# Kernel tuning notes

Hardware: AMD Instinct MI355X
Metric: run time of the kernel (lower is better)

Reference implementation:

```python
import jax, jax.numpy as jnp
import numpy as np

H, I, E, K = 1024, 2816, 8, 2  # hidden, intermediate, n_experts, topk
B, S = 2, 2048


def setup_inputs() -> dict:
    key = jax.random.key(0)
    ks = jax.random.split(key, 6)
    def init(k, shape, fan_in):
        return (jax.random.normal(k, shape, jnp.float32) / np.sqrt(fan_in)).astype(jnp.float32)
    return {
        "x": jax.random.normal(ks[0], (B, S, H), jnp.float32),
        "Wgate": init(ks[1], (H, E), H),   # gating Linear weight (in,out layout)
        "bgate": jnp.zeros((E,), jnp.float32),  # gating Linear bias (nn.Linear default bias=True)
        "Wg": init(ks[2], (E, H, I), H),   # stacked gate_proj, mlp_bias=False
        "Wu": init(ks[3], (E, H, I), H),   # stacked up_proj
        "Wd": init(ks[4], (E, I, H), I),   # stacked down_proj
    }


def reference(x, Wgate, bgate, Wg, Wu, Wd):
    Bb, Ss, Hd = x.shape
    xf = x.reshape(-1, Hd)                       # [N, H] flattened tokens
    logits = xf @ Wgate + bgate                  # [N, E] gate logits
    topv, topi = jax.lax.top_k(logits, K)        # [N, K]
    N = xf.shape[0]
    # sparse combine weights: raw top-k LOGITS (no softmax), zeros elsewhere
    # (faithful to torch: scatter of logits_topk into -inf mask; -inf slots
    #  are never read since only selected experts contribute)
    combine = jnp.zeros_like(logits).at[jnp.arange(N)[:, None], topi].set(topv)  # [N, E]
    # dense grouped SwiGLU over all experts, then sparse combine
    g = jnp.einsum('nh,ehi->nei', xf, Wg)        # [N, E, I]
    u = jnp.einsum('nh,ehi->nei', xf, Wu)        # [N, E, I]
    h = jax.nn.silu(g) * u                       # [N, E, I]
    eo = jnp.einsum('nei,eih->neh', h, Wd)       # [N, E, H]
    out = jnp.einsum('neh,ne->nh', eo, combine).reshape(Bb, Ss, Hd)
    return out, logits
```

## Files before the change

kernel.cpp:

```cpp
#include <hip/hip_runtime.h>

#define HDIM 1024
#define IDIM 2816
#define NEXP 8
#define NTOK 4096
#define NROWS 8192
#define RPAD 8320
#define MAXT 71
#define MAXT64 136
#define GU_NYT 44
#define GU_TG 8
#define GU_NTG 9
#define GU_NWG (GU_NTG * GU_NYT * GU_TG)
#define DN_NWG (MAXT64 * 8)
#define TLDP 130

typedef short bf16x8 __attribute__((ext_vector_type(8)));
typedef float f32x4 __attribute__((ext_vector_type(4)));
typedef unsigned short u16x8 __attribute__((ext_vector_type(8)));

static __device__ __forceinline__ float bf2f(unsigned int u) {
    union { unsigned int i; float f; } v; v.i = u << 16; return v.f;
}
static __device__ __forceinline__ unsigned short f2bf(float f) {
    union { float f; unsigned int i; } v; v.f = f;
    return (unsigned short)((v.i + 0x7fffu + ((v.i >> 16) & 1u)) >> 16);
}

static __device__ __forceinline__ void gload16(const void* g, void* l) {
    __builtin_amdgcn_global_load_lds(
        (const __attribute__((address_space(1))) unsigned int*)g,
        (__attribute__((address_space(3))) unsigned int*)l, 16, 0, 0);
}

__global__ __launch_bounds__(256) void gating_kernel(
    const float* __restrict__ x, const float* __restrict__ Wgate,
    const float* __restrict__ bgate, float* __restrict__ logits_out,
    int* __restrict__ counts, int* __restrict__ topi, float* __restrict__ topv)
{
    int wave = (blockIdx.x << 2) + (threadIdx.x >> 6);
    int lane = threadIdx.x & 63;
    if (wave >= NTOK) return;
    const float* xr = x + (size_t)wave * HDIM;

    double acc[NEXP];
#pragma unroll
    for (int e = 0; e < NEXP; ++e) acc[e] = 0.0;
    for (int it = 0; it < HDIM / 64; ++it) {
        int h = lane + (it << 6);
        float xv = xr[h];
        const float* wr = Wgate + (size_t)h * NEXP;
#pragma unroll
        for (int e = 0; e < NEXP; ++e) acc[e] += (double)xv * (double)wr[e];
    }
#pragma unroll
    for (int e = 0; e < NEXP; ++e) {
        double v = acc[e];
        for (int off = 32; off; off >>= 1) v += __shfl_xor(v, off, 64);
        acc[e] = v + (double)bgate[e];
    }
    float lf[NEXP];
#pragma unroll
    for (int e = 0; e < NEXP; ++e) lf[e] = (float)acc[e];

    if (lane < NEXP) logits_out[(size_t)wave * NEXP + lane] = lf[lane];

    if (lane == 0) {
        int i1 = 0; float v1 = lf[0];
#pragma unroll
        for (int e = 1; e < NEXP; ++e) if (lf[e] > v1) { v1 = lf[e]; i1 = e; }
        int i2 = -1; float v2 = -3.0e38f;
#pragma unroll
        for (int e = 0; e < NEXP; ++e) {
            if (e == i1) continue;
            if (lf[e] > v2) { v2 = lf[e]; i2 = e; }
        }
        topi[wave * 2 + 0] = i1; topv[wave * 2 + 0] = v1;
        topi[wave * 2 + 1] = i2; topv[wave * 2 + 1] = v2;
        atomicAdd(&counts[i1], 1);
        atomicAdd(&counts[i2], 1);
    }
}

__global__ void offsets_kernel(const int* __restrict__ counts,
                               int* __restrict__ offs, int* __restrict__ cursor,
                               int* __restrict__ ntile, int* __restrict__ te,
                               int* __restrict__ tm0,
                               int* __restrict__ ntile64, int* __restrict__ te64,
                               int* __restrict__ tm64)
{
    if (threadIdx.x == 0 && blockIdx.x == 0) {
        int s = 0;
        for (int e = 0; e < NEXP; ++e) { offs[e] = s; cursor[e] = s; s += counts[e]; }
        offs[NEXP] = s;
        int nt = 0, nt64 = 0;
        for (int e = 0; e < NEXP; ++e) {
            int c = counts[e], base = offs[e];
            for (int mt = 0; mt * 128 < c; ++mt) { te[nt] = e; tm0[nt] = base + mt * 128; ++nt; }
            for (int mt = 0; mt * 64 < c; ++mt) { te64[nt64] = e; tm64[nt64] = base + mt * 64; ++nt64; }
        }
        *ntile = nt;
        *ntile64 = nt64;
    }
}

__global__ __launch_bounds__(256) void scatter_kernel(
    const float* __restrict__ x, const int* __restrict__ topi,
    const float* __restrict__ topv, int* __restrict__ cursor,
    float* __restrict__ row_w, int* __restrict__ pos_of,
    unsigned short* __restrict__ Xg)
{
    int p = (blockIdx.x << 2) + (threadIdx.x >> 6);
    int lane = threadIdx.x & 63;
    if (p >= NROWS) return;
    int n = p >> 1;
    int e = topi[p];
    float w = topv[p];
    int pos = 0;
    if (lane == 0) {
        pos = atomicAdd(&cursor[e], 1);
        row_w[pos] = w;
        pos_of[p] = pos;
    }
    pos = __shfl(pos, 0, 64);
    const float* xr = x + (size_t)n * HDIM;
    unsigned short* dst = Xg + (size_t)pos * HDIM;
#pragma unroll
    for (int it = 0; it < HDIM / 256; ++it) {
        int idx = (it * 64 + lane) * 4;
        float4 v = *reinterpret_cast<const float4*>(&xr[idx]);
        ushort4 o;
        o.x = f2bf(v.x); o.y = f2bf(v.y); o.z = f2bf(v.z); o.w = f2bf(v.w);
        *reinterpret_cast<ushort4*>(&dst[idx]) = o;
    }
}

__global__ __launch_bounds__(256) void transpose_gu_kernel(
    const float* __restrict__ Wg, const float* __restrict__ Wu,
    unsigned short* __restrict__ W2)
{
    __shared__ unsigned short lds[128 * TLDP];
    const int kind = blockIdx.z;
    const int e = blockIdx.y;
    const int tt = blockIdx.x;
    const int tr = tt / 22, tc = tt % 22;
    const int tid = threadIdx.x;

    const float* s0 = (kind ? Wu : Wg) + (size_t)e * HDIM * IDIM;
    {
        int r = tid >> 1, ch = (tid & 1) * 64;
        const float* sp = s0 + (size_t)(tr * 128 + r) * IDIM + tc * 128 + ch;
        unsigned short* lp = &lds[r * TLDP + ch];
#pragma unroll
        for (int q = 0; q < 8; ++q) {
            float4 a = *reinterpret_cast<const float4*>(sp + q * 8);
            float4 b = *reinterpret_cast<const float4*>(sp + q * 8 + 4);
            u16x8 o;
            o[0] = f2bf(a.x); o[1] = f2bf(a.y); o[2] = f2bf(a.z); o[3] = f2bf(a.w);
            o[4] = f2bf(b.x); o[5] = f2bf(b.y); o[6] = f2bf(b.z); o[7] = f2bf(b.w);
            *reinterpret_cast<u16x8*>(lp + q * 8) = o;
        }
    }
    __syncthreads();
    {
        const int g = tid & 15;
        unsigned short* d0 = W2 + (size_t)e * 2 * IDIM * HDIM + tr * 128 + g * 8;
#pragma unroll
        for (int cb = 0; cb < 8; ++cb) {
            int c = cb * 16 + (tid >> 4);
            u16x8 o;
#pragma unroll
            for (int jj = 0; jj < 8; ++jj) o[jj] = lds[(g * 8 + jj) * TLDP + c];
            int i = tc * 128 + c;
            int r2 = ((i >> 4) << 5) + (kind << 4) + (i & 15);
            *reinterpret_cast<u16x8*>(d0 + (size_t)r2 * HDIM) = o;
        }
    }
}

__global__ __launch_bounds__(256) void transpose_d_kernel(
    const float* __restrict__ Wd, unsigned short* __restrict__ Wdt)
{
    __shared__ unsigned short lds[128 * TLDP];
    const int e = blockIdx.y;
    const int tt = blockIdx.x;
    const int tr = tt / 8, tc = tt % 8;
    const int tid = threadIdx.x;

    const float* s0 = Wd + (size_t)e * IDIM * HDIM;
    {
        int r = tid >> 1, ch = (tid & 1) * 64;
        const float* sp = s0 + (size_t)(tr * 128 + r) * HDIM + tc * 128 + ch;
        unsigned short* lp = &lds[r * TLDP + ch];
#pragma unroll
        for (int q = 0; q < 8; ++q) {
            float4 a = *reinterpret_cast<const float4*>(sp + q * 8);
            float4 b = *reinterpret_cast<const float4*>(sp + q * 8 + 4);
            u16x8 o;
            o[0] = f2bf(a.x); o[1] = f2bf(a.y); o[2] = f2bf(a.z); o[3] = f2bf(a.w);
            o[4] = f2bf(b.x); o[5] = f2bf(b.y); o[6] = f2bf(b.z); o[7] = f2bf(b.w);
            *reinterpret_cast<u16x8*>(lp + q * 8) = o;
        }
    }
    __syncthreads();
    {
        const int g = tid & 15;
        unsigned short* d0 = Wdt + (size_t)e * HDIM * IDIM + tr * 128 + g * 8;
#pragma unroll
        for (int cb = 0; cb < 8; ++cb) {
            int c = cb * 16 + (tid >> 4);
            u16x8 o;
#pragma unroll
            for (int jj = 0; jj < 8; ++jj) o[jj] = lds[(g * 8 + jj) * TLDP + c];
            *reinterpret_cast<u16x8*>(d0 + (size_t)(tc * 128 + c) * IDIM) = o;
        }
    }
}

__global__ __launch_bounds__(256, 4) void gateup_kernel(
    const unsigned short* __restrict__ Xg,
    const unsigned short* __restrict__ W2,
    const int* __restrict__ offs,
    const int* __restrict__ ntile, const int* __restrict__ te,
    const int* __restrict__ tm0, unsigned short* __restrict__ hbuf)
{
    __shared__ unsigned short As[128 * 64];
    __shared__ unsigned short Bs[128 * 64];

    int bid = blockIdx.x;
    int xcd = bid & 7, rest = bid >> 3;
    int wg = xcd * (GU_NWG / 8) + rest;
    int tg = wg / (GU_NYT * GU_TG);
    int r2 = wg % (GU_NYT * GU_TG);
    int ny = r2 >> 3, ti = r2 & 7;
    int t = tg * GU_TG + ti;
    if (t >= *ntile) return;

    const int e = te[t];
    const int m0 = tm0[t];
    const int r1 = offs[e + 1];
    const int n0 = ny * 128;

    const unsigned short* wb = W2 + (size_t)e * 2 * IDIM * HDIM;

    const int tid = threadIdx.x;
    const int lane = tid & 63, wv = tid >> 6;
    const int wr = (wv >> 1) * 64, wc = (wv & 1) * 64;
    const int lr = lane & 15, kq16 = lane >> 4;

    const int a_row8 = tid >> 3;
    const int a_c16 = tid & 7;

    f32x4 acc[4][4];
#pragma unroll
    for (int m = 0; m < 4; ++m)
#pragma unroll
        for (int n = 0; n < 4; ++n) acc[m][n] = {0.f, 0.f, 0.f, 0.f};

    for (int k0 = 0; k0 < HDIM; k0 += 64) {
        __syncthreads();
#pragma unroll
        for (int ch = 0; ch < 4; ++ch) {
            int row = ch * 32 + a_row8;
            int c16s = a_c16 ^ (row & 7);
            gload16(&Xg[(size_t)(m0 + row) * HDIM + k0 + c16s * 8], &As[ch * 2048 + tid * 8]);
            gload16(&wb[(size_t)(n0 + row) * HDIM + k0 + c16s * 8], &Bs[ch * 2048 + tid * 8]);
        }
        __syncthreads();

#pragma unroll
        for (int ks = 0; ks < 2; ++ks) {
            bf16x8 af[4], bf[4];
#pragma unroll
            for (int m = 0; m < 4; ++m) {
                int row = wr + m * 16 + lr;
                int sw = (ks * 4 + kq16) ^ (row & 7);
                af[m] = *reinterpret_cast<const bf16x8*>(&As[row * 64 + sw * 8]);
            }
#pragma unroll
            for (int n = 0; n < 4; ++n) {
                int row = wc + n * 16 + lr;
                int sw = (ks * 4 + kq16) ^ (row & 7);
                bf[n] = *reinterpret_cast<const bf16x8*>(&Bs[row * 64 + sw * 8]);
            }
#pragma unroll
            for (int m = 0; m < 4; ++m)
#pragma unroll
                for (int n = 0; n < 4; ++n)
                    acc[m][n] = __builtin_amdgcn_mfma_f32_16x16x32_bf16(af[m], bf[n], acc[m][n], 0, 0, 0);
        }
    }

    const int rr = (lane >> 4) * 4;
    const int iloc0 = ((wc >> 5) << 4) + lr;
    const int col0 = ny * 64 + iloc0;
#pragma unroll
    for (int m = 0; m < 4; ++m) {
#pragma unroll
        for (int j = 0; j < 4; ++j) {
            int grow = m0 + wr + m * 16 + rr + j;
            if (grow < r1) {
                unsigned short* hr = &hbuf[(size_t)grow * IDIM + col0];
                float g0 = acc[m][0][j], u0 = acc[m][1][j];
                float g1 = acc[m][2][j], u1 = acc[m][3][j];
                hr[0]  = f2bf(g0 / (1.0f + __expf(-g0)) * u0);
                hr[16] = f2bf(g1 / (1.0f + __expf(-g1)) * u1);
            }
        }
    }
}

__global__ __launch_bounds__(256, 4) void down_kernel(
    const unsigned short* __restrict__ hbuf,
    const unsigned short* __restrict__ Wdt,
    const int* __restrict__ offs,
    const int* __restrict__ ntile64, const int* __restrict__ te64,
    const int* __restrict__ tm64,
    const float* __restrict__ row_w,
    unsigned short* __restrict__ eobuf)
{
    __shared__ unsigned short As[64 * 64];
    __shared__ unsigned short Bs[128 * 64];

    int bid = blockIdx.x;
    int xcd = bid & 7, rest = bid >> 3;
    int ny = rest / 17;
    int t = xcd * 17 + rest % 17;
    if (t >= *ntile64) return;

    const int e = te64[t];
    const int m0 = tm64[t];
    const int r1 = offs[e + 1];
    const int n0 = ny * 128;

    const unsigned short* wd = Wdt + (size_t)e * HDIM * IDIM;

    const int tid = threadIdx.x;
    const int lane = tid & 63, wv = tid >> 6;
    const int wc = wv * 32;
    const int lr = lane & 15, kq16 = lane >> 4;

    const int a_row8 = tid >> 3;
    const int a_c16 = tid & 7;

    f32x4 acc[4][2];
#pragma unroll
    for (int m = 0; m < 4; ++m)
#pragma unroll
        for (int n = 0; n < 2; ++n) acc[m][n] = {0.f, 0.f, 0.f, 0.f};

    for (int k0 = 0; k0 < IDIM; k0 += 64) {
        __syncthreads();
#pragma unroll
        for (int ch = 0; ch < 2; ++ch) {
            int row = ch * 32 + a_row8;
            int c16s = a_c16 ^ (row & 7);
            gload16(&hbuf[(size_t)(m0 + row) * IDIM + k0 + c16s * 8], &As[ch * 2048 + tid * 8]);
        }
#pragma unroll
        for (int ch = 0; ch < 4; ++ch) {
            int row = ch * 32 + a_row8;
            int c16s = a_c16 ^ (row & 7);
            gload16(&wd[(size_t)(n0 + row) * IDIM + k0 + c16s * 8], &Bs[ch * 2048 + tid * 8]);
        }
        __syncthreads();

#pragma unroll
        for (int ks = 0; ks < 2; ++ks) {
            bf16x8 af[4], bf[2];
#pragma unroll
            for (int m = 0; m < 4; ++m) {
                int row = m * 16 + lr;
                int sw = (ks * 4 + kq16) ^ (row & 7);
                af[m] = *reinterpret_cast<const bf16x8*>(&As[row * 64 + sw * 8]);
            }
#pragma unroll
            for (int n = 0; n < 2; ++n) {
                int row = wc + n * 16 + lr;
                int sw = (ks * 4 + kq16) ^ (row & 7);
                bf[n] = *reinterpret_cast<const bf16x8*>(&Bs[row * 64 + sw * 8]);
            }
#pragma unroll
            for (int m = 0; m < 4; ++m)
#pragma unroll
                for (int n = 0; n < 2; ++n)
                    acc[m][n] = __builtin_amdgcn_mfma_f32_16x16x32_bf16(af[m], bf[n], acc[m][n], 0, 0, 0);
        }
    }

    const int rr = (lane >> 4) * 4;
#pragma unroll
    for (int m = 0; m < 4; ++m) {
#pragma unroll
        for (int j = 0; j < 4; ++j) {
            int grow = m0 + m * 16 + rr + j;
            if (grow < r1) {
                float w = row_w[grow];
                unsigned short* er = &eobuf[(size_t)grow * HDIM + n0 + wc + lr];
#pragma unroll
                for (int n = 0; n < 2; ++n)
                    er[n * 16] = f2bf(acc[m][n][j] * w);
            }
        }
    }
}

__global__ __launch_bounds__(256) void combine_kernel(
    const unsigned short* __restrict__ eobuf, const int* __restrict__ pos_of,
    float* __restrict__ out)
{
    int t = blockIdx.x * 256 + threadIdx.x;
    int n = t >> 7;
    int c = (t & 127) << 3;
    int p0 = pos_of[n * 2 + 0];
    int p1 = pos_of[n * 2 + 1];
    uint4 a = *reinterpret_cast<const uint4*>(&eobuf[(size_t)p0 * HDIM + c]);
    uint4 b = *reinterpret_cast<const uint4*>(&eobuf[(size_t)p1 * HDIM + c]);
    float4 o0, o1;
    o0.x = bf2f(a.x & 0xffffu) + bf2f(b.x & 0xffffu);
    o0.y = bf2f(a.x >> 16)     + bf2f(b.x >> 16);
    o0.z = bf2f(a.y & 0xffffu) + bf2f(b.y & 0xffffu);
    o0.w = bf2f(a.y >> 16)     + bf2f(b.y >> 16);
    o1.x = bf2f(a.z & 0xffffu) + bf2f(b.z & 0xffffu);
    o1.y = bf2f(a.z >> 16)     + bf2f(b.z >> 16);
    o1.z = bf2f(a.w & 0xffffu) + bf2f(b.w & 0xffffu);
    o1.w = bf2f(a.w >> 16)     + bf2f(b.w >> 16);
    float* op = out + (size_t)n * HDIM + c;
    *reinterpret_cast<float4*>(op) = o0;
    *reinterpret_cast<float4*>(op + 4) = o1;
}

extern "C" void kernel_launch(void* const* d_in, const int* in_sizes, int n_in,
                              void* d_out, int out_size, void* d_ws, size_t ws_size,
                              hipStream_t stream)
{
    const float* x     = (const float*)d_in[0];
    const float* Wgate = (const float*)d_in[1];
    const float* bgate = (const float*)d_in[2];
    const float* Wg    = (const float*)d_in[3];
    const float* Wu    = (const float*)d_in[4];
    const float* Wd    = (const float*)d_in[5];
    float* out = (float*)d_out;
    float* logits = out + (size_t)NTOK * HDIM;

    char* ws = (char*)d_ws;
    unsigned short* Xg   = (unsigned short*)ws;
    unsigned short* hbuf = (unsigned short*)(ws + 17039360);
    unsigned short* W2   = (unsigned short*)(ws + 63897600);
    char* meta = ws + 156172288;
    int*   counts  = (int*)(meta);
    int*   offs    = (int*)(meta + 64);
    int*   cursor  = (int*)(meta + 128);
    int*   ntile   = (int*)(meta + 192);
    int*   ntile64 = (int*)(meta + 196);
    int*   te      = (int*)(meta + 256);
    int*   tm0     = (int*)(meta + 768);
    int*   te64    = (int*)(meta + 1280);
    int*   tm64    = (int*)(meta + 2048);
    int*   topi    = (int*)(meta + 4096);
    float* topv    = (float*)(meta + 36864);
    float* row_w   = (float*)(meta + 69632);
    int*   pos_of  = (int*)(meta + 102400);

    hipMemsetAsync(counts, 0, 32, stream);

    gating_kernel<<<NTOK / 4, 256, 0, stream>>>(x, Wgate, bgate, logits, counts, topi, topv);
    offsets_kernel<<<1, 64, 0, stream>>>(counts, offs, cursor, ntile, te, tm0,
                                         ntile64, te64, tm64);
    scatter_kernel<<<NROWS / 4, 256, 0, stream>>>(x, topi, topv, cursor, row_w, pos_of, Xg);

    transpose_gu_kernel<<<dim3(176, NEXP, 2), 256, 0, stream>>>(Wg, Wu, W2);

    gateup_kernel<<<GU_NWG, 256, 0, stream>>>(Xg, W2, offs, ntile, te, tm0, hbuf);

    transpose_d_kernel<<<dim3(176, NEXP), 256, 0, stream>>>(Wd, W2);

    down_kernel<<<DN_NWG, 256, 0, stream>>>(hbuf, W2, offs, ntile64, te64, tm64,
                                            row_w, Xg );

    combine_kernel<<<NTOK * HDIM / 8 / 256, 256, 0, stream>>>(Xg, pos_of, out);
}
```

Baseline: 490.8 us.

## Use 128x128 tiles in down-proj GEMM and coalesce transpose tile reads

The down-projection kernel moves from 64-row M tiles to the 128-row tiles already built for gate/up, with a 2x2 wave layout where each wave computes a 64x64 sub-tile. This doubles reuse of each loaded Wd tile per block and halves the number of blocks, which removes the separate 64-row tile list. It also drops the XCD-aware block remap, costs more accumulator registers and LDS, and leaves fewer blocks to fill the GPU. Separately, the weight transpose kernels now read source tiles with fully coalesced float4 accesses spread across rows, replacing the per-thread half-row reads.

```diff
diff --git a/kernel.cpp b/kernel.cpp
--- a/kernel.cpp
+++ b/kernel.cpp
@@ -7,12 +7,11 @@
 #define NROWS 8192
 #define RPAD 8320
 #define MAXT 71
-#define MAXT64 136
 #define GU_NYT 44
 #define GU_TG 8
 #define GU_NTG 9
 #define GU_NWG (GU_NTG * GU_NYT * GU_TG)
-#define DN_NWG (MAXT64 * 8)
+#define DN_NWG (MAXT * 8)
 #define TLDP 130
 
 typedef short bf16x8 __attribute__((ext_vector_type(8)));
@@ -85,22 +84,18 @@
 __global__ void offsets_kernel(const int* __restrict__ counts,
                                int* __restrict__ offs, int* __restrict__ cursor,
                                int* __restrict__ ntile, int* __restrict__ te,
-                               int* __restrict__ tm0,
-                               int* __restrict__ ntile64, int* __restrict__ te64,
-                               int* __restrict__ tm64)
+                               int* __restrict__ tm0)
 {
     if (threadIdx.x == 0 && blockIdx.x == 0) {
         int s = 0;
         for (int e = 0; e < NEXP; ++e) { offs[e] = s; cursor[e] = s; s += counts[e]; }
         offs[NEXP] = s;
-        int nt = 0, nt64 = 0;
+        int nt = 0;
         for (int e = 0; e < NEXP; ++e) {
             int c = counts[e], base = offs[e];
             for (int mt = 0; mt * 128 < c; ++mt) { te[nt] = e; tm0[nt] = base + mt * 128; ++nt; }
-            for (int mt = 0; mt * 64 < c; ++mt) { te64[nt64] = e; tm64[nt64] = base + mt * 64; ++nt64; }
         }
         *ntile = nt;
-        *ntile64 = nt64;
     }
 }
 
@@ -135,6 +130,21 @@
     }
 }
 
+static __device__ __forceinline__ void tp_read_tile(
+    const float* __restrict__ sp, int C, int tid, unsigned short* lds)
+{
+#pragma unroll
+    for (int q = 0; q < 16; ++q) {
+        int idx = q * 1024 + tid * 4;
+        int r = idx >> 7, cc = idx & 127;
+        float4 v = *reinterpret_cast<const float4*>(sp + (size_t)r * C + cc);
+        unsigned w0 = (unsigned)f2bf(v.x) | ((unsigned)f2bf(v.y) << 16);
+        unsigned w1 = (unsigned)f2bf(v.z) | ((unsigned)f2bf(v.w) << 16);
+        unsigned* lp = reinterpret_cast<unsigned*>(&lds[r * TLDP + cc]);
+        lp[0] = w0; lp[1] = w1;
+    }
+}
+
 __global__ __launch_bounds__(256) void transpose_gu_kernel(
     const float* __restrict__ Wg, const float* __restrict__ Wu,
     unsigned short* __restrict__ W2)
@@ -147,20 +157,7 @@
     const int tid = threadIdx.x;
 
     const float* s0 = (kind ? Wu : Wg) + (size_t)e * HDIM * IDIM;
-    {
-        int r = tid >> 1, ch = (tid & 1) * 64;
-        const float* sp = s0 + (size_t)(tr * 128 + r) * IDIM + tc * 128 + ch;
-        unsigned short* lp = &lds[r * TLDP + ch];
-#pragma unroll
-        for (int q = 0; q < 8; ++q) {
-            float4 a = *reinterpret_cast<const float4*>(sp + q * 8);
-            float4 b = *reinterpret_cast<const float4*>(sp + q * 8 + 4);
-            u16x8 o;
-            o[0] = f2bf(a.x); o[1] = f2bf(a.y); o[2] = f2bf(a.z); o[3] = f2bf(a.w);
-            o[4] = f2bf(b.x); o[5] = f2bf(b.y); o[6] = f2bf(b.z); o[7] = f2bf(b.w);
-            *reinterpret_cast<u16x8*>(lp + q * 8) = o;
-        }
-    }
+    tp_read_tile(s0 + (size_t)(tr * 128) * IDIM + tc * 128, IDIM, tid, lds);
     __syncthreads();
     {
         const int g = tid & 15;
@@ -188,20 +185,7 @@
     const int tid = threadIdx.x;
 
     const float* s0 = Wd + (size_t)e * IDIM * HDIM;
-    {
-        int r = tid >> 1, ch = (tid & 1) * 64;
-        const float* sp = s0 + (size_t)(tr * 128 + r) * HDIM + tc * 128 + ch;
-        unsigned short* lp = &lds[r * TLDP + ch];
-#pragma unroll
-        for (int q = 0; q < 8; ++q) {
-            float4 a = *reinterpret_cast<const float4*>(sp + q * 8);
-            float4 b = *reinterpret_cast<const float4*>(sp + q * 8 + 4);
-            u16x8 o;
-            o[0] = f2bf(a.x); o[1] = f2bf(a.y); o[2] = f2bf(a.z); o[3] = f2bf(a.w);
-            o[4] = f2bf(b.x); o[5] = f2bf(b.y); o[6] = f2bf(b.z); o[7] = f2bf(b.w);
-            *reinterpret_cast<u16x8*>(lp + q * 8) = o;
-        }
-    }
+    tp_read_tile(s0 + (size_t)(tr * 128) * HDIM + tc * 128, HDIM, tid, lds);
     __syncthreads();
     {
         const int g = tid & 15;
@@ -314,22 +298,21 @@
     const unsigned short* __restrict__ hbuf,
     const unsigned short* __restrict__ Wdt,
     const int* __restrict__ offs,
-    const int* __restrict__ ntile64, const int* __restrict__ te64,
-    const int* __restrict__ tm64,
+    const int* __restrict__ ntile, const int* __restrict__ te,
+    const int* __restrict__ tm0,
     const float* __restrict__ row_w,
     unsigned short* __restrict__ eobuf)
 {
-    __shared__ unsigned short As[64 * 64];
+    __shared__ unsigned short As[128 * 64];
     __shared__ unsigned short Bs[128 * 64];
 
     int bid = blockIdx.x;
-    int xcd = bid & 7, rest = bid >> 3;
-    int ny = rest / 17;
-    int t = xcd * 17 + rest % 17;
-    if (t >= *ntile64) return;
-
-    const int e = te64[t];
-    const int m0 = tm64[t];
+    int ny = bid & 7;
+    int t = bid >> 3;
+    if (t >= *ntile) return;
+
+    const int e = te[t];
+    const int m0 = tm0[t];
     const int r1 = offs[e + 1];
     const int n0 = ny * 128;
 
@@ -337,45 +320,40 @@
 
     const int tid = threadIdx.x;
     const int lane = tid & 63, wv = tid >> 6;
-    const int wc = wv * 32;
+    const int wr = (wv >> 1) * 64, wc = (wv & 1) * 64;
     const int lr = lane & 15, kq16 = lane >> 4;
 
     const int a_row8 = tid >> 3;
     const int a_c16 = tid & 7;
 
-    f32x4 acc[4][2];
+    f32x4 acc[4][4];
 #pragma unroll
     for (int m = 0; m < 4; ++m)
 #pragma unroll
-        for (int n = 0; n < 2; ++n) acc[m][n] = {0.f, 0.f, 0.f, 0.f};
+        for (int n = 0; n < 4; ++n) acc[m][n] = {0.f, 0.f, 0.f, 0.f};
 
     for (int k0 = 0; k0 < IDIM; k0 += 64) {
         __syncthreads();
 #pragma unroll
-        for (int ch = 0; ch < 2; ++ch) {
+        for (int ch = 0; ch < 4; ++ch) {
             int row = ch * 32 + a_row8;
             int c16s = a_c16 ^ (row & 7);
             gload16(&hbuf[(size_t)(m0 + row) * IDIM + k0 + c16s * 8], &As[ch * 2048 + tid * 8]);
-        }
-#pragma unroll
-        for (int ch = 0; ch < 4; ++ch) {
-            int row = ch * 32 + a_row8;
-            int c16s = a_c16 ^ (row & 7);
             gload16(&wd[(size_t)(n0 + row) * IDIM + k0 + c16s * 8], &Bs[ch * 2048 + tid * 8]);
         }
         __syncthreads();
 
 #pragma unroll
         for (int ks = 0; ks < 2; ++ks) {
-            bf16x8 af[4], bf[2];
+            bf16x8 af[4], bf[4];
 #pragma unroll
             for (int m = 0; m < 4; ++m) {
-                int row = m * 16 + lr;
+                int row = wr + m * 16 + lr;
                 int sw = (ks * 4 + kq16) ^ (row & 7);
                 af[m] = *reinterpret_cast<const bf16x8*>(&As[row * 64 + sw * 8]);
             }
 #pragma unroll
-            for (int n = 0; n < 2; ++n) {
+            for (int n = 0; n < 4; ++n) {
                 int row = wc + n * 16 + lr;
                 int sw = (ks * 4 + kq16) ^ (row & 7);
                 bf[n] = *reinterpret_cast<const bf16x8*>(&Bs[row * 64 + sw * 8]);
@@ -383,7 +361,7 @@
 #pragma unroll
             for (int m = 0; m < 4; ++m)
 #pragma unroll
-                for (int n = 0; n < 2; ++n)
+                for (int n = 0; n < 4; ++n)
                     acc[m][n] = __builtin_amdgcn_mfma_f32_16x16x32_bf16(af[m], bf[n], acc[m][n], 0, 0, 0);
         }
     }
@@ -393,12 +371,12 @@
     for (int m = 0; m < 4; ++m) {
 #pragma unroll
         for (int j = 0; j < 4; ++j) {
-            int grow = m0 + m * 16 + rr + j;
+            int grow = m0 + wr + m * 16 + rr + j;
             if (grow < r1) {
                 float w = row_w[grow];
                 unsigned short* er = &eobuf[(size_t)grow * HDIM + n0 + wc + lr];
 #pragma unroll
-                for (int n = 0; n < 2; ++n)
+                for (int n = 0; n < 4; ++n)
                     er[n * 16] = f2bf(acc[m][n][j] * w);
             }
         }
@@ -452,11 +430,8 @@
     int*   offs    = (int*)(meta + 64);
     int*   cursor  = (int*)(meta + 128);
     int*   ntile   = (int*)(meta + 192);
-    int*   ntile64 = (int*)(meta + 196);
     int*   te      = (int*)(meta + 256);
     int*   tm0     = (int*)(meta + 768);
-    int*   te64    = (int*)(meta + 1280);
-    int*   tm64    = (int*)(meta + 2048);
     int*   topi    = (int*)(meta + 4096);
     float* topv    = (float*)(meta + 36864);
     float* row_w   = (float*)(meta + 69632);
@@ -465,8 +440,7 @@
     hipMemsetAsync(counts, 0, 32, stream);
 
     gating_kernel<<<NTOK / 4, 256, 0, stream>>>(x, Wgate, bgate, logits, counts, topi, topv);
-    offsets_kernel<<<1, 64, 0, stream>>>(counts, offs, cursor, ntile, te, tm0,
-                                         ntile64, te64, tm64);
+    offsets_kernel<<<1, 64, 0, stream>>>(counts, offs, cursor, ntile, te, tm0);
     scatter_kernel<<<NROWS / 4, 256, 0, stream>>>(x, topi, topv, cursor, row_w, pos_of, Xg);
 
     transpose_gu_kernel<<<dim3(176, NEXP, 2), 256, 0, stream>>>(Wg, Wu, W2);
@@ -475,7 +449,7 @@
 
     transpose_d_kernel<<<dim3(176, NEXP), 256, 0, stream>>>(Wd, W2);
 
-    down_kernel<<<DN_NWG, 256, 0, stream>>>(hbuf, W2, offs, ntile64, te64, tm64,
+    down_kernel<<<DN_NWG, 256, 0, stream>>>(hbuf, W2, offs, ntile, te, tm0,
                                             row_w, Xg );
 
     combine_kernel<<<NTOK * HDIM / 8 / 256, 256, 0, stream>>>(Xg, pos_of, out);
```

Result: faster. 478.2 us (-2.6%).
